# Optimization experiments

Hardware: AMD Instinct MI355X
Metric: run time of the kernel (lower is better)

## Reference

```python
import jax, jax.numpy as jnp
import numpy as np

B, L, C1, C2, K, K_IN = 4, 1024, 1024, 1024, 32, 32
BN_EPS = 1e-5


def _gated_bottleneck(x2d, conv_w, conv_b, gamma, beta, lin_w, lin_b):
    # x2d: (N, C1). Grouped 1x1 Conv1d with groups = C1//4: each group maps 4
    # input channels -> 1 output channel.
    n = x2d.shape[0]
    g = conv_w.shape[0]  # bottleneck = C1 // 4
    xc = jnp.einsum('ngf,gf->ng', x2d.reshape(n, g, 4), conv_w) + conv_b
    # BatchNorm1d in training mode: biased batch statistics over N (spatial dim is 1)
    mean = jnp.mean(xc, axis=0)
    var = jnp.mean((xc - mean) ** 2, axis=0)
    xn = (xc - mean) * jax.lax.rsqrt(var + BN_EPS) * gamma + beta
    xa = jax.nn.gelu(xn, approximate=False)  # torch nn.GELU default is exact
    return xa @ lin_w.T + lin_b  # (N, out_features)


def setup_inputs() -> dict:
    key = jax.random.key(0)
    ks = jax.random.split(key, 8)
    g = C1 // 4
    w_std = (2.0 / C2) ** 0.5  # kaiming_normal_ fan_in on (c1, c2)
    lin_std = (1.0 / g) ** 0.5
    return {
        'x': jax.random.normal(ks[0], (B, L, C1), jnp.float32),
        'weight': jax.random.normal(ks[1], (C1, C2), jnp.float32) * w_std,
        'bias': jnp.zeros((C2,), jnp.float32),
        'so_conv_w': jax.random.normal(ks[2], (g, 4), jnp.float32) * 0.5,
        'so_conv_b': jnp.zeros((g,), jnp.float32),
        'so_gamma': jnp.ones((g,), jnp.float32),
        'so_beta': jnp.zeros((g,), jnp.float32),
        'so_lin_w': jax.random.normal(ks[3], (C2, g), jnp.float32) * lin_std,
        'so_lin_b': jnp.zeros((C2,), jnp.float32),
        'si_conv_w': jax.random.normal(ks[4], (g, 4), jnp.float32) * 0.5,
        'si_conv_b': jnp.zeros((g,), jnp.float32),
        'si_gamma': jnp.ones((g,), jnp.float32),
        'si_beta': jnp.zeros((g,), jnp.float32),
        'si_lin_w': jax.random.normal(ks[5], (C1, g), jnp.float32) * lin_std,
        'si_lin_b': jnp.zeros((C1,), jnp.float32),
    }


def reference(x, weight, bias,
              so_conv_w, so_conv_b, so_gamma, so_beta, so_lin_w, so_lin_b,
              si_conv_w, si_conv_b, si_gamma, si_beta, si_lin_w, si_lin_b):
    b, l, c1 = x.shape
    c2 = weight.shape[1]
    x2d = x.reshape(b * l, c1)
    bi = jnp.arange(b)[:, None, None]
    li = jnp.arange(l)[None, :, None]

    # ---- output-sparse branch ----
    score_out = jax.nn.softmax(
        _gated_bottleneck(x2d, so_conv_w, so_conv_b, so_gamma, so_beta,
                          so_lin_w, so_lin_b).reshape(b, l, c2), axis=-1)
    s_v_out, s_i_out = jax.lax.top_k(score_out, K)  # (b,l,K)
    # x . W[:, idx]  ==  (x @ W) gathered at idx; avoids (b,l,c1,K) gather
    full = jnp.einsum('blc,co->blo', x, weight)  # (b,l,c2)
    out_k = jnp.take_along_axis(full, s_i_out, axis=-1) * s_v_out  # (b,l,K)
    out_branch = jnp.zeros((b, l, c2), x.dtype).at[bi, li, s_i_out].add(out_k)

    # ---- input-sparse branch ----
    score_in = jax.nn.softmax(
        _gated_bottleneck(x2d, si_conv_w, si_conv_b, si_gamma, si_beta,
                          si_lin_w, si_lin_b).reshape(b, l, c1), axis=-1)
    s_v_in, s_i_in = jax.lax.top_k(score_in, K_IN)  # (b,l,K_IN)
    x_gated = jnp.take_along_axis(x, s_i_in, axis=-1) * s_v_in  # (b,l,K_IN)
    # sum_k x_gated * W[idx[k], :]  ==  scatter(x_gated) @ W (topk idx unique);
    # avoids materializing (b,l,K_IN,c2) gathered weight rows.
    x_sparse = jnp.zeros((b, l, c1), x.dtype).at[bi, li, s_i_in].add(x_gated)
    in_branch = jnp.einsum('blc,co->blo', x_sparse, weight)

    return out_branch + in_branch + bias
```

## Files before the change

kernel.cpp:

```cpp
#include <hip/hip_runtime.h>
#include <hip/hip_fp16.h>
#include <math.h>


typedef __attribute__((ext_vector_type(8))) short short8;
typedef __attribute__((ext_vector_type(4))) float f32x4;
typedef __attribute__((ext_vector_type(2))) _Float16 half2_t;

__device__ __forceinline__ unsigned int ford(float f) {
    unsigned int b = __float_as_uint(f);
    return (b & 0x80000000u) ? ~b : (b | 0x80000000u);
}

__device__ __forceinline__ unsigned int pkrtz(float a, float b) {
    auto p = __builtin_amdgcn_cvt_pkrtz(a, b);
    return *(const unsigned int*)&p;
}

__global__ __launch_bounds__(256) void prep_k(
    const float* __restrict__ W,
    const float* __restrict__ so_lw, const float* __restrict__ si_lw,
    const float* __restrict__ x,
    const float* __restrict__ so_cw, const float* __restrict__ so_cb,
    const float* __restrict__ si_cw, const float* __restrict__ si_cb,
    __half* __restrict__ wT16, __half* __restrict__ W16,
    unsigned short* __restrict__ whl,
    float* __restrict__ xc, float* __restrict__ partials) {
    int bid = blockIdx.x;
    int t = threadIdx.x;
    if (bid < 1024) {
        __shared__ float tile[32][33];
        int c0 = (bid & 31) * 32, r0 = (bid >> 5) * 32;
        int tx = t & 31, ty = t >> 5;
#pragma unroll
        for (int i = 0; i < 32; i += 8) {
            float v = W[(size_t)(r0 + ty + i) * 1024 + c0 + tx];
            tile[ty + i][tx] = v;
            W16[(size_t)(r0 + ty + i) * 1024 + c0 + tx] = __float2half_rn(v);
        }
        __syncthreads();
#pragma unroll
        for (int i = 0; i < 32; i += 8)
            wT16[(size_t)(c0 + ty + i) * 1024 + r0 + tx] =
                __float2half_rn(tile[tx][ty + i]);
    } else if (bid < 1280) {
        int g = (bid - 1024) * 256 + t;
        int br = g >> 15;
        int rem = g & 32767;
        int ct = rem >> 9;
        int kt = (rem >> 6) & 7;
        int l  = rem & 63;
        int col = ct * 16 + (l & 15);
        int ks  = kt * 32 + (l >> 4) * 8;
        const float* lw = (br ? si_lw : so_lw) + (size_t)col * 256 + ks;
        float4 v0 = *(const float4*)lw;
        float4 v1 = *(const float4*)(lw + 4);
        unsigned hh[8], ll[8];
#pragma unroll
        for (int j = 0; j < 8; ++j) {
            float a = j < 4 ? (&v0.x)[j] : (&v1.x)[j - 4];
            unsigned b = __float_as_uint(a);
            unsigned rh = (b + 0x7FFFu + ((b >> 16) & 1u)) & 0xFFFF0000u;
            hh[j] = rh >> 16;
            float res = a - __uint_as_float(rh);
            unsigned c = __float_as_uint(res);
            unsigned rl = (c + 0x7FFFu + ((c >> 16) & 1u)) & 0xFFFF0000u;
            ll[j] = rl >> 16;
        }
        uint4 ph, pl;
        ph.x = hh[0] | (hh[1] << 16); ph.y = hh[2] | (hh[3] << 16);
        ph.z = hh[4] | (hh[5] << 16); ph.w = hh[6] | (hh[7] << 16);
        pl.x = ll[0] | (ll[1] << 16); pl.y = ll[2] | (ll[3] << 16);
        pl.z = ll[4] | (ll[5] << 16); pl.w = ll[6] | (ll[7] << 16);
        size_t base = (((((size_t)br * 2 + 0) * 64 + ct) * 8 + kt) * 64 + l) * 8;
        size_t hstride = (size_t)64 * 8 * 64 * 8;
        *(uint4*)&whl[base]           = ph;
        *(uint4*)&whl[base + hstride] = pl;
    } else {
        int g = t;
        int n0 = (bid - 1280) * 16;
        float4 wo = ((const float4*)so_cw)[g]; float bo = so_cb[g];
        float4 wi = ((const float4*)si_cw)[g]; float bi = si_cb[g];
        float so_s = 0.f, so_q = 0.f, si_s = 0.f, si_q = 0.f;
#pragma unroll
        for (int r = 0; r < 16; ++r) {
            int n = n0 + r;
            float4 xv = ((const float4*)x)[n * 256 + g];
            float co = fmaf(xv.x, wo.x, fmaf(xv.y, wo.y, fmaf(xv.z, wo.z, fmaf(xv.w, wo.w, bo))));
            float ci = fmaf(xv.x, wi.x, fmaf(xv.y, wi.y, fmaf(xv.z, wi.z, fmaf(xv.w, wi.w, bi))));
            xc[n * 256 + g] = co;
            xc[1048576 + n * 256 + g] = ci;
            so_s += co; so_q += co * co;
            si_s += ci; si_q += ci * ci;
        }
        int b = bid - 1280;
        partials[(b * 4 + 0) * 256 + g] = so_s;
        partials[(b * 4 + 1) * 256 + g] = so_q;
        partials[(b * 4 + 2) * 256 + g] = si_s;
        partials[(b * 4 + 3) * 256 + g] = si_q;
    }
}

__global__ __launch_bounds__(256) void stats_k(
    const float* __restrict__ partials,
    const float* __restrict__ g_so, const float* __restrict__ b_so,
    const float* __restrict__ g_si, const float* __restrict__ b_si,
    float* __restrict__ sc) {
    int g = threadIdx.x;
    int br = blockIdx.x;
    float s = 0.f, q = 0.f;
    for (int b = 0; b < 256; ++b) {
        s += partials[(b * 4 + br * 2 + 0) * 256 + g];
        q += partials[(b * 4 + br * 2 + 1) * 256 + g];
    }
    float mean = s * (1.f / 4096.f);
    float var  = q * (1.f / 4096.f) - mean * mean;
    float rstd = rsqrtf(var + 1e-5f);
    float gm = br ? g_si[g] : g_so[g];
    float bt = br ? b_si[g] : b_so[g];
    float scale = gm * rstd;
    sc[br * 512 + g]       = scale;
    sc[br * 512 + 256 + g] = fmaf(-mean, scale, bt);
}

__global__ __launch_bounds__(256) void gelusplit_k(
    const float* __restrict__ xc, const float* __restrict__ sc,
    unsigned short* __restrict__ xah, unsigned short* __restrict__ xal) {
    int s = blockIdx.x * 256 + threadIdx.x;
    int br  = s >> 17;
    int rem = s & 131071;
    int rtg = rem >> 9;
    int kt  = (rem >> 6) & 7;
    int l   = rem & 63;
    int row = rtg * 16 + (l & 15);
    int ks  = kt * 32 + (l >> 4) * 8;
    const float* xp  = xc + (size_t)br * 1048576 + (size_t)row * 256 + ks;
    const float* scp = sc + br * 512;
    float4 c0 = *(const float4*)xp;
    float4 c1 = *(const float4*)(xp + 4);
    float4 s0 = *(const float4*)(scp + ks);
    float4 s1 = *(const float4*)(scp + ks + 4);
    float4 h0 = *(const float4*)(scp + 256 + ks);
    float4 h1 = *(const float4*)(scp + 256 + ks + 4);
    unsigned hh[8], ll[8];
#pragma unroll
    for (int j = 0; j < 8; ++j) {
        float cv  = j < 4 ? (&c0.x)[j] : (&c1.x)[j - 4];
        float scl = j < 4 ? (&s0.x)[j] : (&s1.x)[j - 4];
        float shf = j < 4 ? (&h0.x)[j] : (&h1.x)[j - 4];
        float z = fmaf(cv, scl, shf);
        float a = 0.5f * z * (1.f + erff(z * 0.70710678f));
        unsigned b = __float_as_uint(a);
        unsigned rh = (b + 0x7FFFu + ((b >> 16) & 1u)) & 0xFFFF0000u;
        hh[j] = rh >> 16;
        float res = a - __uint_as_float(rh);
        unsigned cc = __float_as_uint(res);
        unsigned rl = (cc + 0x7FFFu + ((cc >> 16) & 1u)) & 0xFFFF0000u;
        ll[j] = rl >> 16;
    }
    uint4 ph, pl;
    ph.x = hh[0] | (hh[1] << 16); ph.y = hh[2] | (hh[3] << 16);
    ph.z = hh[4] | (hh[5] << 16); ph.w = hh[6] | (hh[7] << 16);
    pl.x = ll[0] | (ll[1] << 16); pl.y = ll[2] | (ll[3] << 16);
    pl.z = ll[4] | (ll[5] << 16); pl.w = ll[6] | (ll[7] << 16);
    *(uint4*)&xah[(size_t)s * 8] = ph;
    *(uint4*)&xal[(size_t)s * 8] = pl;
}

__global__ __launch_bounds__(256, 2) void logits_mfma2_k(
    const unsigned short* __restrict__ xah, const unsigned short* __restrict__ xal,
    const unsigned short* __restrict__ whl,
    const float* __restrict__ so_lb, const float* __restrict__ si_lb,
    float* __restrict__ logits) {
    int t = threadIdx.x;
    int bx = blockIdx.x;
    int n0 = bx * 64;
    int cb = blockIdx.y;
    int br = blockIdx.z;
    int wave = t >> 6, lane = t & 63;

    f32x4 acc[4][4];
#pragma unroll
    for (int ci = 0; ci < 4; ++ci)
#pragma unroll
        for (int rt = 0; rt < 4; ++rt) acc[ci][rt] = (f32x4){0.f, 0.f, 0.f, 0.f};

    const size_t hstride = (size_t)64 * 8 * 64 * 8;
#pragma unroll 2
    for (int kt = 0; kt < 8; ++kt) {
        short8 Ah[4], Al[4];
#pragma unroll
        for (int rt = 0; rt < 4; ++rt) {
            size_t aoff = (((size_t)br * 256 + bx * 4 + rt) * 8 + kt) * 512 +
                          (size_t)lane * 8;
            Ah[rt] = *(const short8*)&xah[aoff];
            Al[rt] = *(const short8*)&xal[aoff];
        }
#pragma unroll
        for (int ci = 0; ci < 4; ++ci) {
            int ctg = cb * 16 + wave * 4 + ci;
            size_t boff = ((((size_t)br * 2 + 0) * 64 + ctg) * 8 + kt) * 512 +
                          (size_t)lane * 8;
            short8 Wh = *(const short8*)&whl[boff];
            short8 Wl = *(const short8*)&whl[boff + hstride];
#pragma unroll
            for (int rt = 0; rt < 4; ++rt) {
                acc[ci][rt] = __builtin_amdgcn_mfma_f32_16x16x32_bf16(Ah[rt], Wh, acc[ci][rt], 0, 0, 0);
                acc[ci][rt] = __builtin_amdgcn_mfma_f32_16x16x32_bf16(Ah[rt], Wl, acc[ci][rt], 0, 0, 0);
                acc[ci][rt] = __builtin_amdgcn_mfma_f32_16x16x32_bf16(Al[rt], Wh, acc[ci][rt], 0, 0, 0);
            }
        }
    }

    const float* lb = br ? si_lb : so_lb;
#pragma unroll
    for (int ci = 0; ci < 4; ++ci) {
        int colg = cb * 256 + (wave * 4 + ci) * 16 + (lane & 15);
        float lbv = lb[colg];
#pragma unroll
        for (int rt = 0; rt < 4; ++rt) {
#pragma unroll
            for (int i = 0; i < 4; ++i) {
                int row = n0 + rt * 16 + (lane >> 4) * 4 + i;
                logits[((size_t)br * 4096 + row) * 1024 + colg] = acc[ci][rt][i] + lbv;
            }
        }
    }
}

__global__ __launch_bounds__(256) void topkfinal_k(
    const float* __restrict__ logits, const float* __restrict__ x,
    const __half* __restrict__ wT16, const __half* __restrict__ W16,
    const float* __restrict__ bias, float* __restrict__ out) {
    int n = blockIdx.x, t = threadIdx.x, wave = t >> 6, lane = t & 63;
    __shared__ float xr[1024];
    __shared__ float dres[32];
    __shared__ unsigned int gidx[32]; __shared__ float gval[32];
    __shared__ unsigned int iidx[32]; __shared__ float ival[32];
    __shared__ unsigned int hist[2][256];
    __shared__ unsigned int wcnt[2];

    unsigned int xh[8];
    {
        const float4* xg = (const float4*)(x + (size_t)n * 1024);
#pragma unroll
        for (int q = 0; q < 2; ++q) {
            float4 xa = xg[(q * 64 + lane) * 2];
            float4 xb = xg[(q * 64 + lane) * 2 + 1];
            xh[q * 4 + 0] = pkrtz(xa.x, xa.y);
            xh[q * 4 + 1] = pkrtz(xa.z, xa.w);
            xh[q * 4 + 2] = pkrtz(xb.x, xb.y);
            xh[q * 4 + 3] = pkrtz(xb.z, xb.w);
        }
    }

    if (wave < 2) {
        float v[16];
        unsigned int kb[16];
        unsigned int* h = hist[wave];
        const float4* lg = (const float4*)(logits + ((size_t)wave * 4096 + n) * 1024);
#pragma unroll
        for (int q = 0; q < 4; ++q) {
            float4 f = lg[q * 64 + lane];
            v[q * 4 + 0] = f.x; v[q * 4 + 1] = f.y;
            v[q * 4 + 2] = f.z; v[q * 4 + 3] = f.w;
        }
        float rmax = v[0];
#pragma unroll
        for (int i = 1; i < 16; ++i) rmax = fmaxf(rmax, v[i]);
#pragma unroll
        for (int s = 32; s; s >>= 1) rmax = fmaxf(rmax, __shfl_xor(rmax, s));
        float rsum = 0.f;
#pragma unroll
        for (int i = 0; i < 16; ++i) rsum += __expf(v[i] - rmax);
#pragma unroll
        for (int s = 32; s; s >>= 1) rsum += __shfl_xor(rsum, s);
#pragma unroll
        for (int i = 0; i < 16; ++i) kb[i] = ford(v[i]);

        unsigned inmask = 0xFFFFu, need = 32, prefix = 0, lasth = 0;
#pragma unroll
        for (int level = 0; level < 3; ++level) {
            int shift = 24 - level * 8;
            ((uint4*)h)[lane] = make_uint4(0u, 0u, 0u, 0u);
#pragma unroll
            for (int i = 0; i < 16; ++i)
                if ((inmask >> i) & 1u) atomicAdd(&h[(kb[i] >> shift) & 0xFFu], 1u);
            uint4 hv = ((const uint4*)h)[lane];
            unsigned sl = hv.x + hv.y + hv.z + hv.w;
            unsigned S = sl;
#pragma unroll
            for (int off = 1; off < 64; off <<= 1) {
                unsigned o = __shfl_down(S, off);
                if (lane + off < 64) S += o;
            }
            unsigned above = S - sl;
            unsigned cg3 = above + hv.w;
            unsigned cg2 = cg3 + hv.z;
            unsigned cg1 = cg2 + hv.y;
            unsigned cg0 = cg1 + hv.x;
            unsigned pack = 0;
            if      (cg3 >= need) pack = ((4u * lane + 3u) << 12) | cg3;
            else if (cg2 >= need) pack = ((4u * lane + 2u) << 12) | cg2;
            else if (cg1 >= need) pack = ((4u * lane + 1u) << 12) | cg1;
            else if (cg0 >= need) pack = ((4u * lane + 0u) << 12) | cg0;
#pragma unroll
            for (int s = 32; s; s >>= 1) {
                unsigned o = __shfl_xor(pack, s);
                pack = o > pack ? o : pack;
            }
            unsigned bstar = pack >> 12, cstar = pack & 0xFFFu;
            unsigned hstar = h[bstar];
            need -= (cstar - hstar);
            prefix = (prefix << 8) | bstar;
            lasth = hstar;
            unsigned nm = 0;
#pragma unroll
            for (int i = 0; i < 16; ++i)
                if (((inmask >> i) & 1u) && ((kb[i] >> shift) & 0xFFu) == bstar)
                    nm |= 1u << i;
            inmask = nm;
        }

        unsigned winmask = 0;
        if (lasth == need) {
            winmask = inmask;
        } else {
            unsigned avail = inmask;
            unsigned long long best = 0ULL;
#pragma unroll
            for (int i = 0; i < 16; ++i)
                if ((avail >> i) & 1u) {
                    int j = (i >> 2) * 256 + lane * 4 + (i & 3);
                    unsigned long long k64 =
                        ((unsigned long long)kb[i] << 32) | (unsigned int)(~j);
                    best = k64 > best ? k64 : best;
                }
            for (unsigned k = 0; k < need; ++k) {
                unsigned long long w = best;
#pragma unroll
                for (int s = 32; s; s >>= 1) {
                    unsigned long long o = __shfl_xor(w, s);
                    if (o > w) w = o;
                }
                if (best == w) {
                    unsigned long long nb = 0ULL;
#pragma unroll
                    for (int i = 0; i < 16; ++i)
                        if ((avail >> i) & 1u) {
                            int j = (i >> 2) * 256 + lane * 4 + (i & 3);
                            unsigned long long k64 =
                                ((unsigned long long)kb[i] << 32) | (unsigned int)(~j);
                            if (k64 == w) { winmask |= 1u << i; avail &= ~(1u << i); }
                            else nb = k64 > nb ? k64 : nb;
                        }
                    best = nb;
                }
            }
        }
        if (lane == 0) wcnt[wave] = 0;
        unsigned int* oid = wave ? iidx : gidx;
        float*        ovl = wave ? ival : gval;
#pragma unroll
        for (int i = 0; i < 16; ++i) {
            bool wn = ((kb[i] >> 8) > prefix) || ((winmask >> i) & 1u);
            if (wn) {
                unsigned slot = atomicAdd(&wcnt[wave], 1u);
                int j = (i >> 2) * 256 + lane * 4 + (i & 3);
                oid[slot] = (unsigned int)j;
                ovl[slot] = __expf(v[i] - rmax) / rsum;
            }
        }
    }
    __syncthreads();

    if (t < 32) ival[t] *= x[(size_t)n * 1024 + iidx[t]];

#pragma unroll
    for (int d8 = 0; d8 < 8; ++d8) {
        int d = wave * 8 + d8;
        unsigned rowb = (unsigned)__builtin_amdgcn_readfirstlane(gidx[d]);
        const uint4* wrow = (const uint4*)(wT16 + (size_t)rowb * 1024);
        float s = 0.f;
#pragma unroll
        for (int q = 0; q < 2; ++q) {
            uint4 wv = wrow[q * 64 + lane];
            s = __builtin_amdgcn_fdot2(*(const half2_t*)&wv.x,
                                       *(const half2_t*)&xh[q * 4 + 0], s, false);
            s = __builtin_amdgcn_fdot2(*(const half2_t*)&wv.y,
                                       *(const half2_t*)&xh[q * 4 + 1], s, false);
            s = __builtin_amdgcn_fdot2(*(const half2_t*)&wv.z,
                                       *(const half2_t*)&xh[q * 4 + 2], s, false);
            s = __builtin_amdgcn_fdot2(*(const half2_t*)&wv.w,
                                       *(const half2_t*)&xh[q * 4 + 3], s, false);
        }
#pragma unroll
        for (int sft = 32; sft; sft >>= 1) s += __shfl_xor(s, sft);
        if (lane == 0) dres[d] = s * gval[d];
    }
    __syncthreads();

    float4 acc = ((const float4*)bias)[t];
    for (int k = 0; k < 32; ++k) {
        float g = ival[k];
        unsigned c = (unsigned)__builtin_amdgcn_readfirstlane(iidx[k]);
        uint2 wv = ((const uint2*)(W16 + (size_t)c * 1024))[t];
        float2 f0 = __half22float2(*(const __half2*)&wv.x);
        float2 f1 = __half22float2(*(const __half2*)&wv.y);
        acc.x = fmaf(g, f0.x, acc.x); acc.y = fmaf(g, f0.y, acc.y);
        acc.z = fmaf(g, f1.x, acc.z); acc.w = fmaf(g, f1.y, acc.w);
    }
    ((float4*)xr)[t] = acc;
    __syncthreads();
    if (t < 32) xr[gidx[t]] += dres[t];
    __syncthreads();
    ((float4*)(out + (size_t)n * 1024))[t] = ((float4*)xr)[t];
}

extern "C" void kernel_launch(void* const* d_in, const int* in_sizes, int n_in,
                              void* d_out, int out_size, void* d_ws, size_t ws_size,
                              hipStream_t stream) {
    (void)in_sizes; (void)n_in; (void)out_size; (void)ws_size;
    const float* x        = (const float*)d_in[0];
    const float* W        = (const float*)d_in[1];
    const float* bias     = (const float*)d_in[2];
    const float* so_cw    = (const float*)d_in[3];
    const float* so_cb    = (const float*)d_in[4];
    const float* so_gm    = (const float*)d_in[5];
    const float* so_bt    = (const float*)d_in[6];
    const float* so_lw    = (const float*)d_in[7];
    const float* so_lb    = (const float*)d_in[8];
    const float* si_cw    = (const float*)d_in[9];
    const float* si_cb    = (const float*)d_in[10];
    const float* si_gm    = (const float*)d_in[11];
    const float* si_bt    = (const float*)d_in[12];
    const float* si_lw    = (const float*)d_in[13];
    const float* si_lb    = (const float*)d_in[14];
    float* out = (float*)d_out;

    float* ws       = (float*)d_ws;
    __half* wT16    = (__half*)ws;
    __half* W16     = (__half*)(ws + 524288);
    unsigned short* whl = (unsigned short*)(ws + 1048576);
    float* xc       = ws + 1572864;
    float* partials = ws + 3670016;
    float* sc       = ws + 3932160;
    float* logits   = ws + 3933184;
    unsigned short* xah = (unsigned short*)(ws + 12321792);
    unsigned short* xal = (unsigned short*)(ws + 13370368);

    prep_k<<<1536, 256, 0, stream>>>(W, so_lw, si_lw, x, so_cw, so_cb, si_cw, si_cb,
                                     wT16, W16, whl, xc, partials);
    stats_k<<<2, 256, 0, stream>>>(partials, so_gm, so_bt, si_gm, si_bt, sc);
    gelusplit_k<<<1024, 256, 0, stream>>>(xc, sc, xah, xal);
    logits_mfma2_k<<<dim3(64, 4, 2), 256, 0, stream>>>(xah, xal, whl, so_lb, si_lb, logits);
    topkfinal_k<<<4096, 256, 0, stream>>>(logits, x, wT16, W16, bias, out);
}
```

Baseline: 118.0 us.

## Process two rows per block in topk/final kernel so all waves do top-k

The top-k/final kernel now handles two output rows per block. All four waves run the softmax/top-k selection (row × branch) instead of only two waves while the others sit idle. The later dot-product and scatter phases are re-split so each wave covers 16 gathered columns and each thread accumulates 8 output columns. This halves the grid size and uses more LDS per block, which could lower occupancy.

Result: faster. 100.8 us (-14.6%).

```diff
diff --git a/kernel.cpp b/kernel.cpp
--- a/kernel.cpp
+++ b/kernel.cpp
@@ -232,33 +232,23 @@
     const float* __restrict__ logits, const float* __restrict__ x,
     const __half* __restrict__ wT16, const __half* __restrict__ W16,
     const float* __restrict__ bias, float* __restrict__ out) {
-    int n = blockIdx.x, t = threadIdx.x, wave = t >> 6, lane = t & 63;
-    __shared__ float xr[1024];
-    __shared__ float dres[32];
-    __shared__ unsigned int gidx[32]; __shared__ float gval[32];
-    __shared__ unsigned int iidx[32]; __shared__ float ival[32];
-    __shared__ unsigned int hist[2][256];
-    __shared__ unsigned int wcnt[2];
-
-    unsigned int xh[8];
+    int t = threadIdx.x, wave = t >> 6, lane = t & 63;
+    int r0 = blockIdx.x * 2;
+    int ri = wave >> 1;
+    int branch = wave & 1;
+    __shared__ float xr[2][1024];
+    __shared__ float dres[2][32];
+    __shared__ unsigned int gidx[2][32]; __shared__ float gval[2][32];
+    __shared__ unsigned int iidx[2][32]; __shared__ float ival[2][32];
+    __shared__ unsigned int hist[4][256];
+    __shared__ unsigned int wcnt[4];
+
     {
-        const float4* xg = (const float4*)(x + (size_t)n * 1024);
-#pragma unroll
-        for (int q = 0; q < 2; ++q) {
-            float4 xa = xg[(q * 64 + lane) * 2];
-            float4 xb = xg[(q * 64 + lane) * 2 + 1];
-            xh[q * 4 + 0] = pkrtz(xa.x, xa.y);
-            xh[q * 4 + 1] = pkrtz(xa.z, xa.w);
-            xh[q * 4 + 2] = pkrtz(xb.x, xb.y);
-            xh[q * 4 + 3] = pkrtz(xb.z, xb.w);
-        }
-    }
-
-    if (wave < 2) {
         float v[16];
         unsigned int kb[16];
         unsigned int* h = hist[wave];
-        const float4* lg = (const float4*)(logits + ((size_t)wave * 4096 + n) * 1024);
+        const float4* lg =
+            (const float4*)(logits + ((size_t)branch * 4096 + r0 + ri) * 1024);
 #pragma unroll
         for (int q = 0; q < 4; ++q) {
             float4 f = lg[q * 64 + lane];
@@ -359,8 +349,8 @@
             }
         }
         if (lane == 0) wcnt[wave] = 0;
-        unsigned int* oid = wave ? iidx : gidx;
-        float*        ovl = wave ? ival : gval;
+        unsigned int* oid = branch ? iidx[ri] : gidx[ri];
+        float*        ovl = branch ? ival[ri] : gval[ri];
 #pragma unroll
         for (int i = 0; i < 16; ++i) {
             bool wn = ((kb[i] >> 8) > prefix) || ((winmask >> i) & 1u);
@@ -372,14 +362,31 @@
             }
         }
     }
+
+    unsigned int xh[8];
+    {
+        const float4* xg = (const float4*)(x + (size_t)(r0 + ri) * 1024);
+#pragma unroll
+        for (int q = 0; q < 2; ++q) {
+            float4 xa = xg[(q * 64 + lane) * 2];
+            float4 xb = xg[(q * 64 + lane) * 2 + 1];
+            xh[q * 4 + 0] = pkrtz(xa.x, xa.y);
+            xh[q * 4 + 1] = pkrtz(xa.z, xa.w);
+            xh[q * 4 + 2] = pkrtz(xb.x, xb.y);
+            xh[q * 4 + 3] = pkrtz(xb.z, xb.w);
+        }
+    }
     __syncthreads();
 
-    if (t < 32) ival[t] *= x[(size_t)n * 1024 + iidx[t]];
-
-#pragma unroll
-    for (int d8 = 0; d8 < 8; ++d8) {
-        int d = wave * 8 + d8;
-        unsigned rowb = (unsigned)__builtin_amdgcn_readfirstlane(gidx[d]);
+    if (t < 64) {
+        int rr = t >> 5, k = t & 31;
+        ival[rr][k] *= x[(size_t)(r0 + rr) * 1024 + iidx[rr][k]];
+    }
+
+#pragma unroll
+    for (int d8 = 0; d8 < 16; ++d8) {
+        int d = branch * 16 + d8;
+        unsigned rowb = (unsigned)__builtin_amdgcn_readfirstlane(gidx[ri][d]);
         const uint4* wrow = (const uint4*)(wT16 + (size_t)rowb * 1024);
         float s = 0.f;
 #pragma unroll
@@ -396,25 +403,42 @@
         }
 #pragma unroll
         for (int sft = 32; sft; sft >>= 1) s += __shfl_xor(s, sft);
-        if (lane == 0) dres[d] = s * gval[d];
+        if (lane == 0) dres[ri][d] = s * gval[ri][d];
     }
     __syncthreads();
 
-    float4 acc = ((const float4*)bias)[t];
-    for (int k = 0; k < 32; ++k) {
-        float g = ival[k];
-        unsigned c = (unsigned)__builtin_amdgcn_readfirstlane(iidx[k]);
-        uint2 wv = ((const uint2*)(W16 + (size_t)c * 1024))[t];
-        float2 f0 = __half22float2(*(const __half2*)&wv.x);
-        float2 f1 = __half22float2(*(const __half2*)&wv.y);
-        acc.x = fmaf(g, f0.x, acc.x); acc.y = fmaf(g, f0.y, acc.y);
-        acc.z = fmaf(g, f1.x, acc.z); acc.w = fmaf(g, f1.y, acc.w);
-    }
-    ((float4*)xr)[t] = acc;
+    {
+        int rr = t >> 7, j0 = (t & 127) * 8;
+        float4 accA = *(const float4*)&bias[j0];
+        float4 accB = *(const float4*)&bias[j0 + 4];
+        for (int k = 0; k < 32; ++k) {
+            float g = ival[rr][k];
+            unsigned c = (unsigned)__builtin_amdgcn_readfirstlane(iidx[rr][k]);
+            uint4 wv = *(const uint4*)(W16 + (size_t)c * 1024 + j0);
+            float2 f0 = __half22float2(*(const __half2*)&wv.x);
+            float2 f1 = __half22float2(*(const __half2*)&wv.y);
+            float2 f2 = __half22float2(*(const __half2*)&wv.z);
+            float2 f3 = __half22float2(*(const __half2*)&wv.w);
+            accA.x = fmaf(g, f0.x, accA.x); accA.y = fmaf(g, f0.y, accA.y);
+            accA.z = fmaf(g, f1.x, accA.z); accA.w = fmaf(g, f1.y, accA.w);
+            accB.x = fmaf(g, f2.x, accB.x); accB.y = fmaf(g, f2.y, accB.y);
+            accB.z = fmaf(g, f3.x, accB.z); accB.w = fmaf(g, f3.y, accB.w);
+        }
+        *(float4*)&xr[rr][j0]     = accA;
+        *(float4*)&xr[rr][j0 + 4] = accB;
+    }
     __syncthreads();
-    if (t < 32) xr[gidx[t]] += dres[t];
+    if (t < 64) {
+        int rr = t >> 5, d = t & 31;
+        xr[rr][gidx[rr][d]] += dres[rr][d];
+    }
     __syncthreads();
-    ((float4*)(out + (size_t)n * 1024))[t] = ((float4*)xr)[t];
+    {
+        int rr = t >> 7, j0 = (t & 127) * 8;
+        float* op = out + (size_t)(r0 + rr) * 1024 + j0;
+        *(float4*)op       = *(const float4*)&xr[rr][j0];
+        *(float4*)(op + 4) = *(const float4*)&xr[rr][j0 + 4];
+    }
 }
 
 extern "C" void kernel_launch(void* const* d_in, const int* in_sizes, int n_in,
@@ -454,5 +478,5 @@
     stats_k<<<2, 256, 0, stream>>>(partials, so_gm, so_bt, si_gm, si_bt, sc);
     gelusplit_k<<<1024, 256, 0, stream>>>(xc, sc, xah, xal);
     logits_mfma2_k<<<dim3(64, 4, 2), 256, 0, stream>>>(xah, xal, whl, so_lb, si_lb, logits);
-    topkfinal_k<<<4096, 256, 0, stream>>>(logits, x, wT16, W16, bias, out);
-}
+    topkfinal_k<<<2048, 256, 0, stream>>>(logits, x, wT16, W16, bias, out);
+}
```
